# Kernel optimization log

Hardware: AMD Instinct MI355X
Metric: run time of the kernel (lower is better)

The kernel has to match this reference:

```python
import jax, jax.numpy as jnp
import numpy as np

B, N = 2048, 4096

def setup_inputs() -> dict:
    key = jax.random.key(0)
    k1, k2, k3, k4, k5 = jax.random.split(key, 5)
    scale = 1.0 / np.sqrt(N)  # match nn.Linear init scale
    return {
        "t": jnp.zeros((1,), dtype=jnp.float32),
        "y": jax.random.uniform(k1, (B, N), dtype=jnp.float32),
        "W1": jax.random.normal(k2, (N, N), dtype=jnp.float32) * scale,
        "b1": jax.random.normal(k3, (N,), dtype=jnp.float32) * scale,
        "W2": jax.random.normal(k4, (N, N), dtype=jnp.float32) * scale,
        "b2": jax.random.normal(k5, (N,), dtype=jnp.float32) * scale,
    }

def reference(t, y, W1, b1, W2, b2):
    # out = fcc2(fcc1(y)) : two Linear layers (y @ W^T + b)
    h = y @ W1.T + b1            # [B, N]
    out = h @ W2.T + b2          # [B, N]
    # f = ones(N,1) @ y @ out^T  ==  dot(y, out) broadcast over N;
    # dydt = y * (out - dot(y, out))   (replicator equation)
    dot = jnp.sum(y * out, axis=-1, keepdims=True)  # [B, 1]
    return y * (out - dot)       # [B, N]
```

## Files before the change

### kernel.cpp

```cpp
#include <hip/hip_runtime.h>
#include <hip/hip_bf16.h>
#include <stdint.h>

typedef _Float16 f16;
typedef _Float16 f16x4 __attribute__((ext_vector_type(4)));
typedef _Float16 f16x8 __attribute__((ext_vector_type(8)));
typedef float f32x4 __attribute__((ext_vector_type(4)));

#define ASYNC_COPY16(gsrc, ldst)                                                   \
    __builtin_amdgcn_global_load_lds(                                              \
        (__attribute__((address_space(1))) void*)(gsrc),                           \
        (__attribute__((address_space(3))) void*)(ldst), 16, 0, 0)

__global__ __launch_bounds__(256) void cvt_f32_to_f16(const float* __restrict__ in,
                                                      f16* __restrict__ out, int n4) {
    int i = blockIdx.x * 256 + threadIdx.x;
    if (i >= n4) return;
    float4 v = ((const float4*)in)[i];
    f16x4 o;
    o.x = (f16)v.x; o.y = (f16)v.y; o.z = (f16)v.z; o.w = (f16)v.w;
    ((f16x4*)out)[i] = o;
}

__global__ __launch_bounds__(256) void cvt3_f32_to_f16(const float* __restrict__ y,
                                                       const float* __restrict__ W1,
                                                       const float* __restrict__ W2,
                                                       f16* __restrict__ yb,
                                                       f16* __restrict__ w1b,
                                                       f16* __restrict__ w2b,
                                                       int nY4, int nW4) {
    int i = blockIdx.x * 256 + threadIdx.x;
    const float* src;
    f16* dst;
    int off;
    if (i < nY4) {
        src = y; dst = yb; off = i;
    } else if (i < nY4 + nW4) {
        src = W1; dst = w1b; off = i - nY4;
    } else {
        src = W2; dst = w2b; off = i - nY4 - nW4;
        if (off >= nW4) return;
    }
    float4 v = ((const float4*)src)[off];
    f16x4 o;
    o.x = (f16)v.x; o.y = (f16)v.y; o.z = (f16)v.z; o.w = (f16)v.w;
    ((f16x4*)dst)[off] = o;
}

template <int STORE_F16>
__global__ __launch_bounds__(256) void gemm_bt(const f16* __restrict__ A,
                                               const f16* __restrict__ Bm,
                                               const float* __restrict__ bias,
                                               void* __restrict__ Cout,
                                               int M, int N, int K) {
    constexpr int BM = 128, BN = 128, BK = 64;
    __shared__ __align__(16) f16 sA[2][BM * BK];
    __shared__ __align__(16) f16 sB[2][BN * BK];

    const int tid   = threadIdx.x;
    const int lane  = tid & 63;
    const int wave  = tid >> 6;
    const int waveM = wave >> 1;
    const int waveN = wave & 1;

    const int bm = blockIdx.y * BM;
    const int bn = blockIdx.x * BN;

    const f16* Aptr = A + (size_t)bm * K;
    const f16* Bptr = Bm + (size_t)bn * K;

    const int srow_lo = tid >> 3;
    const int sseg    = tid & 7;

    f32x4 acc[4][4] = {};

    const int quad = lane >> 4;
    const int l16  = lane & 15;

    const int iters = K / BK;

    {
#pragma unroll
        for (int j = 0; j < 4; j++) {
            const int row = j * 32 + srow_lo;
            const int seg = sseg ^ (row & 7);
            ASYNC_COPY16(Aptr + (size_t)row * K + 0 + seg * 8, &sA[0][j * 2048 + tid * 8]);
        }
#pragma unroll
        for (int j = 0; j < 4; j++) {
            const int row = j * 32 + srow_lo;
            const int seg = sseg ^ (row & 7);
            ASYNC_COPY16(Bptr + (size_t)row * K + 0 + seg * 8, &sB[0][j * 2048 + tid * 8]);
        }
    }

    int cur = 0;
    for (int it = 0; it < iters; ++it) {
        __builtin_amdgcn_s_waitcnt(0);
        __syncthreads();

        if (it + 1 < iters) {
            const int k0 = (it + 1) * BK;
#pragma unroll
            for (int j = 0; j < 4; j++) {
                const int row = j * 32 + srow_lo;
                const int seg = sseg ^ (row & 7);
                ASYNC_COPY16(Aptr + (size_t)row * K + k0 + seg * 8,
                             &sA[cur ^ 1][j * 2048 + tid * 8]);
            }
#pragma unroll
            for (int j = 0; j < 4; j++) {
                const int row = j * 32 + srow_lo;
                const int seg = sseg ^ (row & 7);
                ASYNC_COPY16(Bptr + (size_t)row * K + k0 + seg * 8,
                             &sB[cur ^ 1][j * 2048 + tid * 8]);
            }
        }

#pragma unroll
        for (int h = 0; h < 2; h++) {
            f16x8 af[4], bf[4];
#pragma unroll
            for (int mi = 0; mi < 4; mi++) {
                const int row = waveM * 64 + mi * 16 + l16;
                const int seg = (h * 4 + quad) ^ (row & 7);
                af[mi] = *(const f16x8*)&sA[cur][row * BK + seg * 8];
            }
#pragma unroll
            for (int ni = 0; ni < 4; ni++) {
                const int row = waveN * 64 + ni * 16 + l16;
                const int seg = (h * 4 + quad) ^ (row & 7);
                bf[ni] = *(const f16x8*)&sB[cur][row * BK + seg * 8];
            }
#pragma unroll
            for (int mi = 0; mi < 4; mi++)
#pragma unroll
                for (int ni = 0; ni < 4; ni++)
                    acc[mi][ni] = __builtin_amdgcn_mfma_f32_16x16x32_f16(af[mi], bf[ni],
                                                                         acc[mi][ni], 0, 0, 0);
        }
        cur ^= 1;
    }

#pragma unroll
    for (int ni = 0; ni < 4; ni++) {
        const int col = bn + waveN * 64 + ni * 16 + l16;
        const float bv = bias[col];
#pragma unroll
        for (int mi = 0; mi < 4; mi++) {
            const int row0 = bm + waveM * 64 + mi * 16 + quad * 4;
#pragma unroll
            for (int r = 0; r < 4; r++) {
                float v = acc[mi][ni][r] + bv;
                if (STORE_F16)
                    ((f16*)Cout)[(size_t)(row0 + r) * N + col] = (f16)v;
                else
                    ((float*)Cout)[(size_t)(row0 + r) * N + col] = v;
            }
        }
    }
}

__global__ __launch_bounds__(256) void replicator(const float* __restrict__ y,
                                                  float* __restrict__ out, int N) {
    const int row = blockIdx.x;
    const float4* y4 = (const float4*)(y + (size_t)row * N);
    float4* o4 = (float4*)(out + (size_t)row * N);
    const int n4 = N / 4;

    float p = 0.f;
    for (int i = threadIdx.x; i < n4; i += 256) {
        float4 a = y4[i], b = o4[i];
        p += a.x * b.x + a.y * b.y + a.z * b.z + a.w * b.w;
    }
#pragma unroll
    for (int off = 32; off > 0; off >>= 1) p += __shfl_down(p, off, 64);

    __shared__ float sred[4];
    if ((threadIdx.x & 63) == 0) sred[threadIdx.x >> 6] = p;
    __syncthreads();
    const float dot = sred[0] + sred[1] + sred[2] + sred[3];

    for (int i = threadIdx.x; i < n4; i += 256) {
        float4 a = y4[i], b = o4[i];
        float4 r;
        r.x = a.x * (b.x - dot);
        r.y = a.y * (b.y - dot);
        r.z = a.z * (b.z - dot);
        r.w = a.w * (b.w - dot);
        o4[i] = r;
    }
}

extern "C" void kernel_launch(void* const* d_in, const int* in_sizes, int n_in,
                              void* d_out, int out_size, void* d_ws, size_t ws_size,
                              hipStream_t stream) {
    const float* y  = (const float*)d_in[1];
    const float* W1 = (const float*)d_in[2];
    const float* b1 = (const float*)d_in[3];
    const float* W2 = (const float*)d_in[4];
    const float* b2 = (const float*)d_in[5];

    const int N = in_sizes[3];
    const int B = in_sizes[1] / N;
    float* out = (float*)d_out;

    const size_t szY = (size_t)B * N;
    const size_t szW = (size_t)N * N;

    const int yn4 = (int)(szY / 4);
    const int wn4 = (int)(szW / 4);

    dim3 g1(N / 128, B / 128);

    const size_t need_big = (szY + 2 * szW + szY) * sizeof(f16);

    if (ws_size >= need_big) {
        f16* yb  = (f16*)d_ws;
        f16* w1b = yb + szY;
        f16* w2b = w1b + szW;
        f16* hb  = w2b + szW;

        const int tot4 = yn4 + 2 * wn4;
        cvt3_f32_to_f16<<<(tot4 + 255) / 256, 256, 0, stream>>>(y, W1, W2, yb, w1b, w2b,
                                                                yn4, wn4);
        gemm_bt<1><<<g1, 256, 0, stream>>>(yb, w1b, b1, hb, B, N, N);
        gemm_bt<0><<<g1, 256, 0, stream>>>(hb, w2b, b2, out, B, N, N);
    } else {
        f16* yb = (f16*)d_ws;
        f16* wb = yb + szY;
        f16* hb = wb + szW;

        cvt_f32_to_f16<<<yn4 / 256, 256, 0, stream>>>(y, yb, yn4);
        cvt_f32_to_f16<<<wn4 / 256, 256, 0, stream>>>(W1, wb, wn4);
        gemm_bt<1><<<g1, 256, 0, stream>>>(yb, wb, b1, hb, B, N, N);
        cvt_f32_to_f16<<<wn4 / 256, 256, 0, stream>>>(W2, wb, wn4);
        gemm_bt<0><<<g1, 256, 0, stream>>>(hb, wb, b2, out, B, N, N);
    }

    replicator<<<B, 256, 0, stream>>>(y, out, N);
}
```

Before: 371.4 us.

## Use triple-buffered 128x256 GEMM tiles with 8 waves and interleaved loads

Each GEMM block grows to 128x256 tiles with 512 threads (8 waves in a 2x4 grid). The LDS pipeline moves from double to triple buffering, prefetching two K-steps ahead. Async global-to-LDS copies are split across the two half-K MFMA phases, with partial vmcnt waits, barriers and s_setprio around MFMA bursts. The aim is better overlap of memory and compute and more reuse of the A tile, at the cost of more LDS per block (one block per CU) and a grid of only 256 blocks.

```diff
diff --git a/kernel.cpp b/kernel.cpp
--- a/kernel.cpp
+++ b/kernel.cpp
@@ -48,20 +48,20 @@
 }
 
 template <int STORE_F16>
-__global__ __launch_bounds__(256) void gemm_bt(const f16* __restrict__ A,
-                                               const f16* __restrict__ Bm,
-                                               const float* __restrict__ bias,
-                                               void* __restrict__ Cout,
-                                               int M, int N, int K) {
-    constexpr int BM = 128, BN = 128, BK = 64;
-    __shared__ __align__(16) f16 sA[2][BM * BK];
-    __shared__ __align__(16) f16 sB[2][BN * BK];
+__global__ __launch_bounds__(512, 1) void gemm_bt(const f16* __restrict__ A,
+                                                  const f16* __restrict__ Bm,
+                                                  const float* __restrict__ bias,
+                                                  void* __restrict__ Cout,
+                                                  int M, int N, int K) {
+    constexpr int BM = 128, BN = 256, BK = 64;
+    __shared__ __align__(16) f16 sA[3][BM * BK];
+    __shared__ __align__(16) f16 sB[3][BN * BK];
 
     const int tid   = threadIdx.x;
     const int lane  = tid & 63;
     const int wave  = tid >> 6;
-    const int waveM = wave >> 1;
-    const int waveN = wave & 1;
+    const int waveM = wave >> 2;
+    const int waveN = wave & 3;
 
     const int bm = blockIdx.y * BM;
     const int bn = blockIdx.x * BN;
@@ -69,8 +69,27 @@
     const f16* Aptr = A + (size_t)bm * K;
     const f16* Bptr = Bm + (size_t)bn * K;
 
-    const int srow_lo = tid >> 3;
-    const int sseg    = tid & 7;
+    const int srow = tid >> 3;
+    const int sseg = tid & 7;
+
+    const f16* gA[2];
+    const f16* gB[4];
+#pragma unroll
+    for (int s = 0; s < 2; s++) {
+        const int row = s * 64 + srow;
+        const int seg = sseg ^ (row & 7);
+        gA[s] = Aptr + (size_t)row * K + seg * 8;
+    }
+#pragma unroll
+    for (int s = 0; s < 4; s++) {
+        const int row = s * 64 + srow;
+        const int seg = sseg ^ (row & 7);
+        gB[s] = Bptr + (size_t)row * K + seg * 8;
+    }
+    const int ldst = tid * 8;
+
+#define STAGE_A(s, buf, k0) ASYNC_COPY16(gA[s] + (k0), &sA[buf][(s)*4096 + ldst])
+#define STAGE_B(s, buf, k0) ASYNC_COPY16(gB[s] + (k0), &sB[buf][(s)*4096 + ldst])
 
     f32x4 acc[4][4] = {};
 
@@ -79,68 +98,97 @@
 
     const int iters = K / BK;
 
-    {
-#pragma unroll
-        for (int j = 0; j < 4; j++) {
-            const int row = j * 32 + srow_lo;
-            const int seg = sseg ^ (row & 7);
-            ASYNC_COPY16(Aptr + (size_t)row * K + 0 + seg * 8, &sA[0][j * 2048 + tid * 8]);
-        }
-#pragma unroll
-        for (int j = 0; j < 4; j++) {
-            const int row = j * 32 + srow_lo;
-            const int seg = sseg ^ (row & 7);
-            ASYNC_COPY16(Bptr + (size_t)row * K + 0 + seg * 8, &sB[0][j * 2048 + tid * 8]);
-        }
-    }
-
-    int cur = 0;
-    for (int it = 0; it < iters; ++it) {
-        __builtin_amdgcn_s_waitcnt(0);
-        __syncthreads();
-
-        if (it + 1 < iters) {
-            const int k0 = (it + 1) * BK;
-#pragma unroll
-            for (int j = 0; j < 4; j++) {
-                const int row = j * 32 + srow_lo;
-                const int seg = sseg ^ (row & 7);
-                ASYNC_COPY16(Aptr + (size_t)row * K + k0 + seg * 8,
-                             &sA[cur ^ 1][j * 2048 + tid * 8]);
-            }
-#pragma unroll
-            for (int j = 0; j < 4; j++) {
-                const int row = j * 32 + srow_lo;
-                const int seg = sseg ^ (row & 7);
-                ASYNC_COPY16(Bptr + (size_t)row * K + k0 + seg * 8,
-                             &sB[cur ^ 1][j * 2048 + tid * 8]);
-            }
-        }
-
-#pragma unroll
-        for (int h = 0; h < 2; h++) {
+#pragma unroll
+    for (int s = 0; s < 2; s++) STAGE_A(s, 0, 0);
+#pragma unroll
+    for (int s = 0; s < 4; s++) STAGE_B(s, 0, 0);
+#pragma unroll
+    for (int s = 0; s < 2; s++) STAGE_A(s, 1, BK);
+#pragma unroll
+    for (int s = 0; s < 4; s++) STAGE_B(s, 1, BK);
+    asm volatile("s_waitcnt vmcnt(6)" ::: "memory");
+    __builtin_amdgcn_s_barrier();
+
+    int cbuf = 0;
+    for (int t = 0; t < iters; ++t) {
+        const int pbuf = (cbuf >= 1) ? cbuf - 1 : 2;
+        const bool st  = (t + 2 < iters);
+        const int k0   = (t + 2) * BK;
+
+        {
             f16x8 af[4], bf[4];
 #pragma unroll
             for (int mi = 0; mi < 4; mi++) {
                 const int row = waveM * 64 + mi * 16 + l16;
-                const int seg = (h * 4 + quad) ^ (row & 7);
-                af[mi] = *(const f16x8*)&sA[cur][row * BK + seg * 8];
+                const int seg = (0 * 4 + quad) ^ (row & 7);
+                af[mi] = *(const f16x8*)&sA[cbuf][row * BK + seg * 8];
             }
 #pragma unroll
             for (int ni = 0; ni < 4; ni++) {
                 const int row = waveN * 64 + ni * 16 + l16;
-                const int seg = (h * 4 + quad) ^ (row & 7);
-                bf[ni] = *(const f16x8*)&sB[cur][row * BK + seg * 8];
-            }
+                const int seg = (0 * 4 + quad) ^ (row & 7);
+                bf[ni] = *(const f16x8*)&sB[cbuf][row * BK + seg * 8];
+            }
+            if (st) {
+                STAGE_A(0, pbuf, k0);
+                STAGE_A(1, pbuf, k0);
+                STAGE_B(0, pbuf, k0);
+            }
+            __builtin_amdgcn_s_barrier();
+            asm volatile("s_waitcnt lgkmcnt(0)" ::: "memory");
+            __builtin_amdgcn_s_setprio(1);
 #pragma unroll
             for (int mi = 0; mi < 4; mi++)
 #pragma unroll
                 for (int ni = 0; ni < 4; ni++)
                     acc[mi][ni] = __builtin_amdgcn_mfma_f32_16x16x32_f16(af[mi], bf[ni],
                                                                          acc[mi][ni], 0, 0, 0);
+            __builtin_amdgcn_s_setprio(0);
+            __builtin_amdgcn_s_barrier();
         }
-        cur ^= 1;
-    }
+
+        {
+            f16x8 af[4], bf[4];
+#pragma unroll
+            for (int mi = 0; mi < 4; mi++) {
+                const int row = waveM * 64 + mi * 16 + l16;
+                const int seg = (1 * 4 + quad) ^ (row & 7);
+                af[mi] = *(const f16x8*)&sA[cbuf][row * BK + seg * 8];
+            }
+#pragma unroll
+            for (int ni = 0; ni < 4; ni++) {
+                const int row = waveN * 64 + ni * 16 + l16;
+                const int seg = (1 * 4 + quad) ^ (row & 7);
+                bf[ni] = *(const f16x8*)&sB[cbuf][row * BK + seg * 8];
+            }
+            if (st) {
+                STAGE_B(1, pbuf, k0);
+                STAGE_B(2, pbuf, k0);
+                STAGE_B(3, pbuf, k0);
+            }
+            __builtin_amdgcn_s_barrier();
+            asm volatile("s_waitcnt lgkmcnt(0)" ::: "memory");
+            __builtin_amdgcn_s_setprio(1);
+#pragma unroll
+            for (int mi = 0; mi < 4; mi++)
+#pragma unroll
+                for (int ni = 0; ni < 4; ni++)
+                    acc[mi][ni] = __builtin_amdgcn_mfma_f32_16x16x32_f16(af[mi], bf[ni],
+                                                                         acc[mi][ni], 0, 0, 0);
+            __builtin_amdgcn_s_setprio(0);
+            if (st) {
+                asm volatile("s_waitcnt vmcnt(6)" ::: "memory");
+            } else {
+                asm volatile("s_waitcnt vmcnt(0)" ::: "memory");
+            }
+            __builtin_amdgcn_s_barrier();
+        }
+
+        cbuf = (cbuf >= 2) ? 0 : cbuf + 1;
+    }
+
+#undef STAGE_A
+#undef STAGE_B
 
 #pragma unroll
     for (int ni = 0; ni < 4; ni++) {
@@ -211,7 +259,7 @@
     const int yn4 = (int)(szY / 4);
     const int wn4 = (int)(szW / 4);
 
-    dim3 g1(N / 128, B / 128);
+    dim3 g1(N / 256, B / 128);
 
     const size_t need_big = (szY + 2 * szW + szY) * sizeof(f16);
 
@@ -224,8 +272,8 @@
         const int tot4 = yn4 + 2 * wn4;
         cvt3_f32_to_f16<<<(tot4 + 255) / 256, 256, 0, stream>>>(y, W1, W2, yb, w1b, w2b,
                                                                 yn4, wn4);
-        gemm_bt<1><<<g1, 256, 0, stream>>>(yb, w1b, b1, hb, B, N, N);
-        gemm_bt<0><<<g1, 256, 0, stream>>>(hb, w2b, b2, out, B, N, N);
+        gemm_bt<1><<<g1, 512, 0, stream>>>(yb, w1b, b1, hb, B, N, N);
+        gemm_bt<0><<<g1, 512, 0, stream>>>(hb, w2b, b2, out, B, N, N);
     } else {
         f16* yb = (f16*)d_ws;
         f16* wb = yb + szY;
@@ -233,9 +281,9 @@
 
         cvt_f32_to_f16<<<yn4 / 256, 256, 0, stream>>>(y, yb, yn4);
         cvt_f32_to_f16<<<wn4 / 256, 256, 0, stream>>>(W1, wb, wn4);
-        gemm_bt<1><<<g1, 256, 0, stream>>>(yb, wb, b1, hb, B, N, N);
+        gemm_bt<1><<<g1, 512, 0, stream>>>(yb, wb, b1, hb, B, N, N);
         cvt_f32_to_f16<<<wn4 / 256, 256, 0, stream>>>(W2, wb, wn4);
-        gemm_bt<0><<<g1, 256, 0, stream>>>(hb, wb, b2, out, B, N, N);
+        gemm_bt<0><<<g1, 512, 0, stream>>>(hb, wb, b2, out, B, N, N);
     }
 
     replicator<<<B, 256, 0, stream>>>(y, out, N);
```

After: 350.3 us. -5.7%, faster.

## Use 512-thread GEMM blocks with 2x4 wave grid and smaller per-wave tiles

Applied to the files above, without the earlier changes.

The GEMM kernel now launches 512 threads (8 waves) per 128x128 tile instead of 256, arranged 2x4, so each wave computes a 64x32 sub-tile with 8 accumulators instead of 16. Global-to-LDS staging is split across more threads with precomputed source pointers, and launch bounds request higher occupancy. The aim is more waves in flight to hide memory and LDS latency. In exchange, each wave does less MFMA work per LDS fragment load, which lowers register reuse and adds more barrier participants.

```diff
diff --git a/kernel.cpp b/kernel.cpp
--- a/kernel.cpp
+++ b/kernel.cpp
@@ -11,6 +11,8 @@
     __builtin_amdgcn_global_load_lds(                                              \
         (__attribute__((address_space(1))) void*)(gsrc),                           \
         (__attribute__((address_space(3))) void*)(ldst), 16, 0, 0)
+
+#define MFMA16(a, b, c) __builtin_amdgcn_mfma_f32_16x16x32_f16((a), (b), (c), 0, 0, 0)
 
 __global__ __launch_bounds__(256) void cvt_f32_to_f16(const float* __restrict__ in,
                                                       f16* __restrict__ out, int n4) {
@@ -48,11 +50,11 @@
 }
 
 template <int STORE_F16>
-__global__ __launch_bounds__(256) void gemm_bt(const f16* __restrict__ A,
-                                               const f16* __restrict__ Bm,
-                                               const float* __restrict__ bias,
-                                               void* __restrict__ Cout,
-                                               int M, int N, int K) {
+__global__ __launch_bounds__(512, 4) void gemm_bt(const f16* __restrict__ A,
+                                                  const f16* __restrict__ Bm,
+                                                  const float* __restrict__ bias,
+                                                  void* __restrict__ Cout,
+                                                  int M, int N, int K) {
     constexpr int BM = 128, BN = 128, BK = 64;
     __shared__ __align__(16) f16 sA[2][BM * BK];
     __shared__ __align__(16) f16 sB[2][BN * BK];
@@ -60,8 +62,8 @@
     const int tid   = threadIdx.x;
     const int lane  = tid & 63;
     const int wave  = tid >> 6;
-    const int waveM = wave >> 1;
-    const int waveN = wave & 1;
+    const int waveM = wave >> 2;
+    const int waveN = wave & 3;
 
     const int bm = blockIdx.y * BM;
     const int bn = blockIdx.x * BN;
@@ -69,82 +71,78 @@
     const f16* Aptr = A + (size_t)bm * K;
     const f16* Bptr = Bm + (size_t)bn * K;
 
-    const int srow_lo = tid >> 3;
-    const int sseg    = tid & 7;
-
-    f32x4 acc[4][4] = {};
+    const int srow = tid >> 3;
+    const int sseg = tid & 7;
+
+    const f16* gA[2];
+    const f16* gB[2];
+#pragma unroll
+    for (int s = 0; s < 2; s++) {
+        const int row = s * 64 + srow;
+        const int seg = sseg ^ (row & 7);
+        gA[s] = Aptr + (size_t)row * K + seg * 8;
+        gB[s] = Bptr + (size_t)row * K + seg * 8;
+    }
+    const int ldst = tid * 8;
+
+#define STAGE_A(s, buf, k0) ASYNC_COPY16(gA[s] + (k0), &sA[buf][(s)*4096 + ldst])
+#define STAGE_B(s, buf, k0) ASYNC_COPY16(gB[s] + (k0), &sB[buf][(s)*4096 + ldst])
+
+    f32x4 acc[4][2] = {};
 
     const int quad = lane >> 4;
     const int l16  = lane & 15;
 
     const int iters = K / BK;
 
-    {
-#pragma unroll
-        for (int j = 0; j < 4; j++) {
-            const int row = j * 32 + srow_lo;
-            const int seg = sseg ^ (row & 7);
-            ASYNC_COPY16(Aptr + (size_t)row * K + 0 + seg * 8, &sA[0][j * 2048 + tid * 8]);
-        }
-#pragma unroll
-        for (int j = 0; j < 4; j++) {
-            const int row = j * 32 + srow_lo;
-            const int seg = sseg ^ (row & 7);
-            ASYNC_COPY16(Bptr + (size_t)row * K + 0 + seg * 8, &sB[0][j * 2048 + tid * 8]);
-        }
-    }
+#pragma unroll
+    for (int s = 0; s < 2; s++) STAGE_A(s, 0, 0);
+#pragma unroll
+    for (int s = 0; s < 2; s++) STAGE_B(s, 0, 0);
 
     int cur = 0;
-    for (int it = 0; it < iters; ++it) {
+    for (int t = 0; t < iters; ++t) {
         __builtin_amdgcn_s_waitcnt(0);
         __syncthreads();
 
-        if (it + 1 < iters) {
-            const int k0 = (it + 1) * BK;
-#pragma unroll
-            for (int j = 0; j < 4; j++) {
-                const int row = j * 32 + srow_lo;
-                const int seg = sseg ^ (row & 7);
-                ASYNC_COPY16(Aptr + (size_t)row * K + k0 + seg * 8,
-                             &sA[cur ^ 1][j * 2048 + tid * 8]);
-            }
-#pragma unroll
-            for (int j = 0; j < 4; j++) {
-                const int row = j * 32 + srow_lo;
-                const int seg = sseg ^ (row & 7);
-                ASYNC_COPY16(Bptr + (size_t)row * K + k0 + seg * 8,
-                             &sB[cur ^ 1][j * 2048 + tid * 8]);
-            }
+        if (t + 1 < iters) {
+            const int k0 = (t + 1) * BK;
+#pragma unroll
+            for (int s = 0; s < 2; s++) STAGE_A(s, cur ^ 1, k0);
+#pragma unroll
+            for (int s = 0; s < 2; s++) STAGE_B(s, cur ^ 1, k0);
         }
 
 #pragma unroll
         for (int h = 0; h < 2; h++) {
-            f16x8 af[4], bf[4];
+            f16x8 af[4], bf[2];
 #pragma unroll
             for (int mi = 0; mi < 4; mi++) {
                 const int row = waveM * 64 + mi * 16 + l16;
-                const int seg = (h * 4 + quad) ^ (row & 7);
+                const int seg = (h * 4 + quad) ^ (l16 & 7);
                 af[mi] = *(const f16x8*)&sA[cur][row * BK + seg * 8];
             }
 #pragma unroll
-            for (int ni = 0; ni < 4; ni++) {
-                const int row = waveN * 64 + ni * 16 + l16;
-                const int seg = (h * 4 + quad) ^ (row & 7);
+            for (int ni = 0; ni < 2; ni++) {
+                const int row = waveN * 32 + ni * 16 + l16;
+                const int seg = (h * 4 + quad) ^ (l16 & 7);
                 bf[ni] = *(const f16x8*)&sB[cur][row * BK + seg * 8];
             }
 #pragma unroll
             for (int mi = 0; mi < 4; mi++)
 #pragma unroll
-                for (int ni = 0; ni < 4; ni++)
-                    acc[mi][ni] = __builtin_amdgcn_mfma_f32_16x16x32_f16(af[mi], bf[ni],
-                                                                         acc[mi][ni], 0, 0, 0);
+                for (int ni = 0; ni < 2; ni++)
+                    acc[mi][ni] = MFMA16(af[mi], bf[ni], acc[mi][ni]);
         }
         cur ^= 1;
     }
 
-#pragma unroll
-    for (int ni = 0; ni < 4; ni++) {
-        const int col = bn + waveN * 64 + ni * 16 + l16;
+#undef STAGE_A
+#undef STAGE_B
+
+#pragma unroll
+    for (int ni = 0; ni < 2; ni++) {
+        const int col = bn + waveN * 32 + ni * 16 + l16;
         const float bv = bias[col];
 #pragma unroll
         for (int mi = 0; mi < 4; mi++) {
@@ -224,8 +222,8 @@
         const int tot4 = yn4 + 2 * wn4;
         cvt3_f32_to_f16<<<(tot4 + 255) / 256, 256, 0, stream>>>(y, W1, W2, yb, w1b, w2b,
                                                                 yn4, wn4);
-        gemm_bt<1><<<g1, 256, 0, stream>>>(yb, w1b, b1, hb, B, N, N);
-        gemm_bt<0><<<g1, 256, 0, stream>>>(hb, w2b, b2, out, B, N, N);
+        gemm_bt<1><<<g1, 512, 0, stream>>>(yb, w1b, b1, hb, B, N, N);
+        gemm_bt<0><<<g1, 512, 0, stream>>>(hb, w2b, b2, out, B, N, N);
     } else {
         f16* yb = (f16*)d_ws;
         f16* wb = yb + szY;
@@ -233,9 +231,9 @@
 
         cvt_f32_to_f16<<<yn4 / 256, 256, 0, stream>>>(y, yb, yn4);
         cvt_f32_to_f16<<<wn4 / 256, 256, 0, stream>>>(W1, wb, wn4);
-        gemm_bt<1><<<g1, 256, 0, stream>>>(yb, wb, b1, hb, B, N, N);
+        gemm_bt<1><<<g1, 512, 0, stream>>>(yb, wb, b1, hb, B, N, N);
         cvt_f32_to_f16<<<wn4 / 256, 256, 0, stream>>>(W2, wb, wn4);
-        gemm_bt<0><<<g1, 256, 0, stream>>>(hb, wb, b2, out, B, N, N);
+        gemm_bt<0><<<g1, 512, 0, stream>>>(hb, wb, b2, out, B, N, N);
     }
 
     replicator<<<B, 256, 0, stream>>>(y, out, N);
```

Measured after the change: 353.2 us. 1.05x faster.
